# Optimization experiments

Measured on AMD Instinct MI355X. Metric: run time of the kernel, lower is better.

The kernel has to match this reference:

```python
import jax, jax.numpy as jnp
import numpy as np

N_DIST, H, W, K = 256, 256, 192, 129
DR, DR0, DELTA = 0.2, 0.2, 1e-11


def _dual_exp(d, b1, b2, b3, b4):
    return b1 * np.exp(-b2 * d) + b3 * np.exp(-b4 * d)


def setup_inputs() -> dict:
    key = jax.random.key(0)
    d = (np.arange(N_DIST) + 1.0) * DR                      # distances (cm)
    gaus_amp = _dual_exp(d, 1.0, 0.01, 0.1, 0.001)
    gaus_sig = 0.05 * d + 1.0
    bkg_amp = _dual_exp(d, 0.05, 0.05, 0.01, 0.005)
    bkg_sig = 0.08 * d + 2.0
    xk = np.arange(-(K // 2), K // 2 + 1) * DR / DR0        # (K,) kernel coords
    # gaussian kernel (get_gaus_layer)
    kernel_g = np.sqrt(gaus_amp)[:, None] * np.exp(-xk[None, :] ** 2 / (2 * gaus_sig[:, None] ** 2 + DELTA))
    # background kernels (get_bkg_layers) with emulated splines
    w_f = lambda t: np.exp(-np.abs(t))
    iso_f = lambda t: 1.0 / (1.0 + t ** 2)
    xw = xk[None, :] / bkg_sig[:, None]
    kernel_w = bkg_amp[:, None] * (DR / DR0) * w_f(xw)
    kernel_iso = bkg_amp[:, None] * (DR / DR0) * iso_f(xw)
    # normalization factor (configure)
    xs = np.linspace(-5.0, 5.0, 2001)
    Iw = np.trapz(w_f(xs), xs)
    Iiso = np.trapz(iso_f(xs), xs)
    Nw = 3 * bkg_amp * Iw * bkg_sig
    Niso = bkg_amp * Iiso * bkg_sig
    Ng2 = gaus_amp * 2 * np.pi * gaus_sig ** 2 * (DR0 / DR) ** 2
    norm = (Nw + Niso ** 2 + 1.0) * Ng2
    x = jax.random.uniform(key, (1, N_DIST, H, W), dtype=jnp.float32)
    return {
        "x": x,
        "kernel_g": jnp.asarray(kernel_g, jnp.float32),
        "kernel_w": jnp.asarray(kernel_w, jnp.float32),
        "kernel_iso": jnp.asarray(kernel_iso, jnp.float32),
        "norm": jnp.asarray(norm, jnp.float32),
    }


def _dwconv(x, kern, axis):
    """Depthwise 'same' Conv1d along `axis` of (N,H,W); channels = dim 0."""
    n = x.shape[0]
    perm = (2, 0, 1) if axis == 1 else (1, 0, 2)   # -> (batch, channels=N, length)
    inv = (1, 2, 0) if axis == 1 else (1, 0, 2)
    xb = jnp.transpose(x, perm)
    y = jax.lax.conv_general_dilated(
        xb, kern[:, None, :], (1,), 'SAME',
        feature_group_count=n, dimension_numbers=('NCH', 'OIH', 'NCH'))
    return jnp.transpose(y, inv)


def _rotate(x, ang):
    """Bilinear rotation of (N,S,S) in dims (1,2), zero padding (grid_sample-like)."""
    s = x.shape[1]
    c = (s - 1) * 0.5
    ca, sa = jnp.cos(ang), jnp.sin(ang)
    idx = jnp.arange(s, dtype=x.dtype) - c
    yy, xx = jnp.meshgrid(idx, idx, indexing='ij')
    sy = ca * yy + sa * xx + c   # inverse-rotated source coords
    sx = -sa * yy + ca * xx + c
    y0 = jnp.floor(sy)
    x0 = jnp.floor(sx)
    fy, fx = sy - y0, sx - x0
    y0i, x0i = y0.astype(jnp.int32), x0.astype(jnp.int32)

    def gat(yi, xi):
        valid = (yi >= 0) & (yi < s) & (xi >= 0) & (xi < s)
        v = x[:, jnp.clip(yi, 0, s - 1), jnp.clip(xi, 0, s - 1)]
        return jnp.where(valid, v, 0.0)

    return (gat(y0i, x0i) * (1 - fy) * (1 - fx)
            + gat(y0i, x0i + 1) * (1 - fy) * fx
            + gat(y0i + 1, x0i) * fy * (1 - fx)
            + gat(y0i + 1, x0i + 1) * fy * fx)


def reference(x, kernel_g, kernel_w, kernel_iso, norm):
    out = x[0]                                   # (N, H, W)
    out = _dwconv(out, kernel_g, 1)
    out = _dwconv(out, kernel_g, 2)
    iso = _dwconv(out, kernel_iso, 1)
    iso = _dwconv(iso, kernel_iso, 2)
    n, h, w = out.shape
    pad = (n - w) // 2
    padded = jnp.pad(out, ((0, 0), (0, 0), (pad, pad)))  # (N, H, H) square plane
    tails = jnp.zeros_like(padded)
    for i in range(3):                            # 0, 60, 120 degrees
        ang = float(np.deg2rad(60 * i))
        t = _rotate(padded, ang)
        t = _dwconv(t, kernel_w, 2)
        tails = tails + _rotate(t, -ang)
    tails = tails[:, :, pad:pad + w]
    out = (out + tails + iso) / norm[:, None, None]
    return out[None]
```

## Files before the change

kernel.cpp:

```cpp
#include <hip/hip_runtime.h>
#include <cmath>

#define CN   256
#define HN   256
#define WN   192
#define KN   129
#define RN   64
#define SN   256
#define PADN 32

#define BBR 92
#define BBP 96

template <int TW, int WD, bool ACC>
__global__ __launch_bounds__(512, 2) void conv_w_lds(const float* __restrict__ in,
                                                     const float* __restrict__ kern,
                                                     float* __restrict__ out) {
    constexpr int NO    = TW / 8;
    constexpr int TWW   = TW + 128;
    constexpr int PITCH = TWW + 1;
    constexpr int NB    = (2 * NO + 31) / NO;
    __shared__ float lds[64 * PITCH + 132];
    float* __restrict__ ldsK = lds + 64 * PITCH;
    const int tid = threadIdx.x;
    const int x0  = blockIdx.x * TW;
    const int h0  = blockIdx.y * 64;
    const int c   = blockIdx.z;
    const float* __restrict__ in_c = in + ((size_t)c * HN + h0) * WD;

    if (tid < 132) ldsK[tid] = (tid < KN) ? kern[c * KN + tid] : 0.f;

    const int colg = tid & 63;
    const int rr   = tid >> 6;
    const int off  = x0 - 64;

    if (off >= 0 && off + TWW <= WD) {
#pragma unroll
        for (int m = 0; m < 4; ++m) {
            if (colg + 64 * m < TWW) {
#pragma unroll
                for (int k = 0; k < 8; ++k)
                    lds[(rr + 8 * k) * PITCH + colg + 64 * m] =
                        in_c[(size_t)(rr + 8 * k) * WD + off + colg + 64 * m];
            }
        }
    } else {
#pragma unroll
        for (int m = 0; m < 4; ++m) {
            if (colg + 64 * m < TWW) {
#pragma unroll
                for (int k = 0; k < 8; ++k) {
                    int g  = off + colg + 64 * m;
                    int gc = min(max(g, 0), WD - 1);
                    float v = in_c[(size_t)(rr + 8 * k) * WD + gc];
                    lds[(rr + 8 * k) * PITCH + colg + 64 * m] = (g == gc) ? v : 0.f;
                }
            }
        }
    }
    __syncthreads();

    const int wv = tid >> 6;
    const int l  = tid & 63;
    const int base = l * PITCH + wv * NO;

    float acc[NO];
#pragma unroll
    for (int t = 0; t < NO; ++t) acc[t] = 0.f;

    float H[4][NO];
    const float4* __restrict__ k4 = (const float4*)ldsK;
#pragma unroll
    for (int s = 0; s < 4; ++s) {
        const int sb = base + 32 * s;
#pragma unroll
        for (int k = 0; k < NB - 1; ++k)
#pragma unroll
            for (int i = 0; i < NO; ++i) H[k][i] = lds[sb + k * NO + i];
        float4 kc = k4[8 * s];
#pragma unroll
        for (int q = 0; q < 8; ++q) {
            float4 kn = (q < 7) ? k4[8 * s + q + 1] : kc;
#pragma unroll
            for (int u = 0; u < 4; ++u) {
                const int up = 4 * q + u;
                const float kj = (u == 0) ? kc.x : (u == 1) ? kc.y
                               : (u == 2) ? kc.z : kc.w;
#pragma unroll
                for (int t = 0; t < NO; ++t) {
                    const int e = up + t;
                    const float val = (e < NO)     ? H[0][e]
                                    : (e < 2 * NO) ? H[1][e - NO]
                                    : (e < 3 * NO) ? H[2][e - 2 * NO]
                                                   : H[3][e - 3 * NO];
                    acc[t] = fmaf(val, kj, acc[t]);
                }
            }
            if (q == 0) {
#pragma unroll
                for (int i = 0; i < NO; ++i)
                    H[NB - 1][i] = lds[sb + (NB - 1) * NO + i];
            }
            kc = kn;
        }
        if (s == 3) {
            const float k128 = ldsK[128];
#pragma unroll
            for (int t = 0; t < NO; ++t) {
                const int e = 32 + t;
                const float val = (e < NO)     ? H[0][e]
                                : (e < 2 * NO) ? H[1][e - NO]
                                : (e < 3 * NO) ? H[2][e - 2 * NO]
                                               : H[3][e - 3 * NO];
                acc[t] = fmaf(val, k128, acc[t]);
            }
        }
    }

    __syncthreads();
#pragma unroll
    for (int i = 0; i < NO; ++i) lds[base + i] = acc[i];
    __syncthreads();
    float* __restrict__ obase = out + ((size_t)c * HN + h0) * WD + x0;
#pragma unroll
    for (int k = 0; k < (64 * TW) / 512; ++k) {
        const int idx = k * 512 + tid;
        const int r  = idx / TW;
        const int cl = idx - r * TW;
        float v = lds[r * PITCH + cl];
        if (ACC) v += obase[(size_t)r * WD + cl];
        obase[(size_t)r * WD + cl] = v;
    }
}

__global__ __launch_bounds__(512, 2) void conv_h_lds(const float* __restrict__ in,
                                                     const float* __restrict__ kern,
                                                     float* __restrict__ out) {
    __shared__ float lds[256 * 64 + 132];
    float* __restrict__ ldsK = lds + 256 * 64;
    const int tid = threadIdx.x;
    const int x0  = blockIdx.x * 64;
    const int h0  = blockIdx.y * 128;
    const int c   = blockIdx.z;
    const float* __restrict__ in_c = in + (size_t)c * HN * WN + x0;

    if (tid < 132) ldsK[tid] = (tid < KN) ? kern[c * KN + tid] : 0.f;

    {
        const int f4 = (tid & 15) * 4;
        const int rw = tid >> 4;
        const int off = h0 - 64;
#pragma unroll
        for (int p = 0; p < 8; ++p) {
            const int lr = rw + 32 * p;
            const int g  = off + lr;
            const int gc = min(max(g, 0), HN - 1);
            float4 v = *(const float4*)(in_c + (size_t)gc * WN + f4);
            if (g != gc) { v.x = 0.f; v.y = 0.f; v.z = 0.f; v.w = 0.f; }
            *(float4*)(lds + lr * 64 + f4) = v;
        }
    }
    __syncthreads();

    const int W = (tid >> 6) * 16;
    const int l = tid & 63;

    float acc[16];
#pragma unroll
    for (int t = 0; t < 16; ++t) acc[t] = 0.f;

    float X0[16], X1[16], X2[16], X3[16];

#define RD16(BUF, b)                                                          \
    { _Pragma("unroll")                                                       \
      for (int i = 0; i < 16; ++i) BUF[i] = lds[(W + 16 * (b) + i) * 64 + l]; }

#define STG(s, LOW, MID, HIGH, NXT, hasNxt)                                   \
    {                                                                         \
        const float4* __restrict__ k4 = (const float4*)ldsK;                  \
        float4 kc = k4[8 * (s)];                                              \
        _Pragma("unroll")                                                     \
        for (int q = 0; q < 8; ++q) {                                         \
            float4 kn = (q < 7) ? k4[8 * (s) + q + 1] : kc;                   \
            _Pragma("unroll")                                                 \
            for (int u = 0; u < 4; ++u) {                                     \
                const float kj = (u == 0) ? kc.x : (u == 1) ? kc.y            \
                               : (u == 2) ? kc.z : kc.w;                      \
                _Pragma("unroll")                                             \
                for (int t = 0; t < 16; ++t) {                                \
                    const int e = 4 * q + u + t;                              \
                    const float val = (e < 16) ? LOW[e]                       \
                                    : (e < 32) ? MID[e - 16] : HIGH[e - 32];  \
                    acc[t] = fmaf(val, kj, acc[t]);                           \
                }                                                             \
            }                                                                 \
            if (q == 0) RD16(HIGH, 2 * (s) + 2)                               \
            if ((hasNxt) && q == 1) RD16(NXT, 2 * (s) + 3)                    \
            kc = kn;                                                          \
        }                                                                     \
    }

    RD16(X0, 0)
    RD16(X1, 1)
    STG(0, X0, X1, X2, X3, true)
    STG(1, X2, X3, X0, X1, true)
    STG(2, X0, X1, X2, X3, true)
    STG(3, X2, X3, X0, X1, false)
#undef RD16
#undef STG

    {
        const float k128 = ldsK[128];
#pragma unroll
        for (int t = 0; t < 16; ++t) acc[t] = fmaf(X0[t], k128, acc[t]);
    }

    float* __restrict__ ob = out + ((size_t)c * HN + h0 + W) * WN + x0 + l;
#pragma unroll
    for (int t = 0; t < 16; ++t) ob[(size_t)t * WN] = acc[t];
}

__global__ __launch_bounds__(256) void rot_fwd_lds(const float* __restrict__ Cin,
                                                   float* __restrict__ out,
                                                   float ca, float sa) {
    __shared__ float tile[BBR * BBP];
    const int j0 = blockIdx.x * 64;
    const int i0 = blockIdx.y * 64;
    const int c  = blockIdx.z;
    const float cc = (SN - 1) * 0.5f;
    const float yA = (float)i0 - cc, yB = (float)(i0 + 63) - cc;
    const float xA = (float)j0 - cc, xB = (float)(j0 + 63) - cc;
    const float syAA = ca * yA + sa * xA + cc, syAB = ca * yA + sa * xB + cc;
    const float syBA = ca * yB + sa * xA + cc, syBB = ca * yB + sa * xB + cc;
    const float sxAA = -sa * yA + ca * xA + cc, sxAB = -sa * yA + ca * xB + cc;
    const float sxBA = -sa * yB + ca * xA + cc, sxBB = -sa * yB + ca * xB + cc;
    const int ybase = (int)floorf(fminf(fminf(syAA, syAB), fminf(syBA, syBB))) - 1;
    const int xbase = (int)floorf(fminf(fminf(sxAA, sxAB), fminf(sxBA, sxBB))) - 1;

    const float* __restrict__ base = Cin + (size_t)c * HN * WN;
    for (int t = threadIdx.x; t < BBR * BBP; t += 256) {
        const int r  = t / BBP;
        const int q  = t - r * BBP;
        const int gy = ybase + r;
        const int gx = xbase + q - PADN;
        float v = 0.f;
        if ((unsigned)gy < (unsigned)HN && (unsigned)gx < (unsigned)WN)
            v = base[(size_t)gy * WN + gx];
        tile[t] = v;
    }
    __syncthreads();

    const int l  = threadIdx.x & 63;
    const int r0 = threadIdx.x >> 6;
    const int j  = j0 + l;
    const float xx = (float)j - cc;
    float* __restrict__ ocol = out + (size_t)c * SN * SN + j;
#pragma unroll
    for (int t = 0; t < 16; ++t) {
        const int i = i0 + r0 + 4 * t;
        const float yy = (float)i - cc;
        const float sy = ca * yy + sa * xx + cc;
        const float sx = -sa * yy + ca * xx + cc;
        const float y0f = floorf(sy), x0f = floorf(sx);
        const float fy = sy - y0f, fx = sx - x0f;
        const int ly = (int)y0f - ybase;
        const int lx = (int)x0f - xbase;
        const float* p = tile + ly * BBP + lx;
        const float v00 = p[0], v01 = p[1], v10 = p[BBP], v11 = p[BBP + 1];
        ocol[(size_t)i * SN] = (1.f - fy) * ((1.f - fx) * v00 + fx * v01)
                             + fy * ((1.f - fx) * v10 + fx * v11);
    }
}

template <bool FINAL>
__global__ __launch_bounds__(256) void rot_bwd_lds(const float* __restrict__ U,
                                                   float* __restrict__ dst,
                                                   const float* __restrict__ accIn,
                                                   const float* __restrict__ norm,
                                                   float ca, float sa) {
    __shared__ float tile[BBR * BBP];
    const int x0 = blockIdx.x * 64;
    const int i0 = blockIdx.y * 64;
    const int c  = blockIdx.z;
    const float cc = (SN - 1) * 0.5f;
    const float yA = (float)i0 - cc, yB = (float)(i0 + 63) - cc;
    const float xA = (float)(x0 + PADN) - cc, xB = (float)(x0 + PADN + 63) - cc;
    const float syAA = ca * yA + sa * xA + cc, syAB = ca * yA + sa * xB + cc;
    const float syBA = ca * yB + sa * xA + cc, syBB = ca * yB + sa * xB + cc;
    const float sxAA = -sa * yA + ca * xA + cc, sxAB = -sa * yA + ca * xB + cc;
    const float sxBA = -sa * yB + ca * xA + cc, sxBB = -sa * yB + ca * xB + cc;
    const int ybase = (int)floorf(fminf(fminf(syAA, syAB), fminf(syBA, syBB))) - 1;
    const int xbase = (int)floorf(fminf(fminf(sxAA, sxAB), fminf(sxBA, sxBB))) - 1;

    const float* __restrict__ base = U + (size_t)c * SN * SN;
    for (int t = threadIdx.x; t < BBR * BBP; t += 256) {
        const int r  = t / BBP;
        const int q  = t - r * BBP;
        const int gy = ybase + r;
        const int gx = xbase + q;
        float v = 0.f;
        if ((unsigned)gy < (unsigned)SN && (unsigned)gx < (unsigned)SN)
            v = base[(size_t)gy * SN + gx];
        tile[t] = v;
    }
    __syncthreads();

    const int l  = threadIdx.x & 63;
    const int r0 = threadIdx.x >> 6;
    const int xc = x0 + l;
    const float xx = (float)(xc + PADN) - cc;
    float inv = 0.f;
    if constexpr (FINAL) inv = 1.f / norm[c];
#pragma unroll
    for (int t = 0; t < 16; ++t) {
        const int i = i0 + r0 + 4 * t;
        const float yy = (float)i - cc;
        const float sy = ca * yy + sa * xx + cc;
        const float sx = -sa * yy + ca * xx + cc;
        const float y0f = floorf(sy), x0f = floorf(sx);
        const float fy = sy - y0f, fx = sx - x0f;
        const int ly = (int)y0f - ybase;
        const int lx = (int)x0f - xbase;
        const float* p = tile + ly * BBP + lx;
        const float v00 = p[0], v01 = p[1], v10 = p[BBP], v11 = p[BBP + 1];
        const float val = (1.f - fy) * ((1.f - fx) * v00 + fx * v01)
                        + fy * ((1.f - fx) * v10 + fx * v11);
        const size_t idx = ((size_t)c * HN + i) * WN + xc;
        if constexpr (FINAL) {
            dst[idx] = (dst[idx] + accIn[idx] + val) * inv;
        } else {
            dst[idx] += val;
        }
    }
}

extern "C" void kernel_launch(void* const* d_in, const int* in_sizes, int n_in,
                              void* d_out, int out_size, void* d_ws, size_t ws_size,
                              hipStream_t stream) {
    const float* x    = (const float*)d_in[0];
    const float* kg   = (const float*)d_in[1];
    const float* kw   = (const float*)d_in[2];
    const float* kiso = (const float*)d_in[3];
    const float* norm = (const float*)d_in[4];

    float* C = (float*)d_out;
    float* ws = (float*)d_ws;
    const size_t IMG = (size_t)CN * HN * WN;
    const size_t PSQ = (size_t)CN * SN * SN;
    float* B   = ws;
    float* acc = ws + IMG;
    float* T   = ws + 2 * IMG;
    float* U   = T + PSQ;

    const dim3 blk256(256);
    const dim3 blk512(512);
    const dim3 convHGrid(WN / 64, HN / 128, CN);
    const dim3 convW192Grid(2, HN / 64, CN);
    const dim3 convW256Grid(2, HN / 64, CN);
    const dim3 rotFGrid(SN / 64, SN / 64, CN);
    const dim3 rotBGrid(WN / 64, HN / 64, CN);

    conv_h_lds<<<convHGrid, blk512, 0, stream>>>(x, kg, B);
    conv_w_lds<96, WN, false><<<convW192Grid, blk512, 0, stream>>>(B, kg, C);
    conv_h_lds<<<convHGrid, blk512, 0, stream>>>(C, kiso, B);
    conv_w_lds<96, WN, false><<<convW192Grid, blk512, 0, stream>>>(B, kiso, acc);
    conv_w_lds<96, WN, true><<<convW192Grid, blk512, 0, stream>>>(C, kw, acc);
    const double a1 = 60.0 * M_PI / 180.0, a2 = 120.0 * M_PI / 180.0;
    const float c1 = (float)cos(a1), s1 = (float)sin(a1);
    const float c2 = (float)cos(a2), s2 = (float)sin(a2);

    rot_fwd_lds<<<rotFGrid, blk256, 0, stream>>>(C, T, c1, s1);
    conv_w_lds<128, SN, false><<<convW256Grid, blk512, 0, stream>>>(T, kw, U);
    rot_bwd_lds<false><<<rotBGrid, blk256, 0, stream>>>(U, acc, nullptr, nullptr, c1, -s1);

    rot_fwd_lds<<<rotFGrid, blk256, 0, stream>>>(C, T, c2, s2);
    conv_w_lds<128, SN, false><<<convW256Grid, blk512, 0, stream>>>(T, kw, U);
    rot_bwd_lds<true><<<rotBGrid, blk256, 0, stream>>>(U, C, acc, norm, c2, -s2);

    (void)in_sizes; (void)n_in; (void)out_size; (void)ws_size;
}
```

Measured before the change: 705.9 us.

## Restructure width conv into full-row tiles with sliding 8-wide register window

The width-direction depthwise conv now loads a fixed 192-column window per 64-row tile with float4 LDS stores. It handles zero padding at register-fill time rather than staging a halo, and streams input through an 8x8 rotating register window instead of reloading 4 blocks per kernel segment. The 192-wide image convs switch to one block covering the full width, halving the grid and eliminating redundant halo loads. Output writes and the accumulate path become float4. This trades fewer blocks and more register pressure for less LDS and global traffic.

```diff
diff --git a/kernel.cpp b/kernel.cpp
--- a/kernel.cpp
+++ b/kernel.cpp
@@ -17,9 +17,12 @@
                                                      const float* __restrict__ kern,
                                                      float* __restrict__ out) {
     constexpr int NO    = TW / 8;
-    constexpr int TWW   = TW + 128;
-    constexpr int PITCH = TWW + 1;
-    constexpr int NB    = (2 * NO + 31) / NO;
+    constexpr int NBLK  = (NO + 32) / 8;
+    constexpr int TOTB  = (NO + 128) / 8;
+    constexpr int RC    = 192;
+    constexpr int PITCH = 196;
+    static_assert(NO == 16 || NO == 24, "unsupported TW");
+    static_assert(TW == WD || 2 * TW == WD, "grid.x must be edge tiles only");
     __shared__ float lds[64 * PITCH + 132];
     float* __restrict__ ldsK = lds + 64 * PITCH;
     const int tid = threadIdx.x;
@@ -30,106 +33,114 @@
 
     if (tid < 132) ldsK[tid] = (tid < KN) ? kern[c * KN + tid] : 0.f;
 
-    const int colg = tid & 63;
-    const int rr   = tid >> 6;
-    const int off  = x0 - 64;
-
-    if (off >= 0 && off + TWW <= WD) {
-#pragma unroll
-        for (int m = 0; m < 4; ++m) {
-            if (colg + 64 * m < TWW) {
-#pragma unroll
-                for (int k = 0; k < 8; ++k)
-                    lds[(rr + 8 * k) * PITCH + colg + 64 * m] =
-                        in_c[(size_t)(rr + 8 * k) * WD + off + colg + 64 * m];
-            }
-        }
-    } else {
-#pragma unroll
-        for (int m = 0; m < 4; ++m) {
-            if (colg + 64 * m < TWW) {
-#pragma unroll
-                for (int k = 0; k < 8; ++k) {
-                    int g  = off + colg + 64 * m;
-                    int gc = min(max(g, 0), WD - 1);
-                    float v = in_c[(size_t)(rr + 8 * k) * WD + gc];
-                    lds[(rr + 8 * k) * PITCH + colg + 64 * m] = (g == gc) ? v : 0.f;
+    const int gc0 = max(0, x0 - 64);
+    {
+        const int srow = tid >> 3;
+        const int scg  = tid & 7;
+#pragma unroll
+        for (int m = 0; m < 6; ++m) {
+            const int c4 = scg + 8 * m;
+            *(float4*)(lds + srow * PITCH + 4 * c4) =
+                *(const float4*)(in_c + (size_t)srow * WD + gc0 + 4 * c4);
+        }
+    }
+    __syncthreads();
+
+    const int wv  = tid >> 6;
+    const int l   = tid & 63;
+    const int ac0 = x0 + wv * NO - 64;
+    const int lbase = l * PITCH + (ac0 - gc0);
+
+    float acc[NO];
+#pragma unroll
+    for (int t = 0; t < NO; ++t) acc[t] = 0.f;
+
+    float X[8][8];
+
+#define RD8(G)                                                                \
+    if ((G) < TOTB) {                                                         \
+        const int ac_ = ac0 + 8 * (G);                                        \
+        if (ac_ >= 0 && ac_ + 8 <= WD) {             \
+            const float4 a_ = *(const float4*)(lds + lbase + 8 * (G));        \
+            const float4 b_ = *(const float4*)(lds + lbase + 8 * (G) + 4);    \
+            X[(G) & 7][0] = a_.x; X[(G) & 7][1] = a_.y;                       \
+            X[(G) & 7][2] = a_.z; X[(G) & 7][3] = a_.w;                       \
+            X[(G) & 7][4] = b_.x; X[(G) & 7][5] = b_.y;                       \
+            X[(G) & 7][6] = b_.z; X[(G) & 7][7] = b_.w;                       \
+        } else {                                                              \
+            _Pragma("unroll")                                                 \
+            for (int i_ = 0; i_ < 8; ++i_) {                                  \
+                const int cc_ = ac_ + i_;                                     \
+                const int cl_ = min(max(cc_, 0), WD - 1);                     \
+                const float v_ = lds[l * PITCH + (cl_ - gc0)];                \
+                X[(G) & 7][i_] = (cc_ == cl_) ? v_ : 0.f;                     \
+            }                                                                 \
+        }                                                                     \
+    }
+
+    RD8(0) RD8(1) RD8(2) RD8(3) RD8(4) RD8(5)
+    if (NBLK == 7) { RD8(6) }
+
+    const float4* __restrict__ k4 = (const float4*)ldsK;
+#pragma unroll
+    for (int s = 0; s < 4; ++s) {
+        float4 kc = k4[8 * s];
+#pragma unroll
+        for (int q = 0; q < 8; ++q) {
+            float4 kn = (q < 7) ? k4[8 * s + q + 1] : kc;
+#pragma unroll
+            for (int u = 0; u < 4; ++u) {
+                const float kj = (u == 0) ? kc.x : (u == 1) ? kc.y
+                               : (u == 2) ? kc.z : kc.w;
+#pragma unroll
+                for (int t = 0; t < NO; ++t) {
+                    const int e = 4 * q + u + t;
+                    acc[t] = fmaf(X[(4 * s + e / 8) & 7][e & 7], kj, acc[t]);
                 }
             }
-        }
-    }
-    __syncthreads();
-
-    const int wv = tid >> 6;
-    const int l  = tid & 63;
-    const int base = l * PITCH + wv * NO;
-
-    float acc[NO];
-#pragma unroll
-    for (int t = 0; t < NO; ++t) acc[t] = 0.f;
-
-    float H[4][NO];
-    const float4* __restrict__ k4 = (const float4*)ldsK;
-#pragma unroll
-    for (int s = 0; s < 4; ++s) {
-        const int sb = base + 32 * s;
-#pragma unroll
-        for (int k = 0; k < NB - 1; ++k)
-#pragma unroll
-            for (int i = 0; i < NO; ++i) H[k][i] = lds[sb + k * NO + i];
-        float4 kc = k4[8 * s];
-#pragma unroll
-        for (int q = 0; q < 8; ++q) {
-            float4 kn = (q < 7) ? k4[8 * s + q + 1] : kc;
-#pragma unroll
-            for (int u = 0; u < 4; ++u) {
-                const int up = 4 * q + u;
-                const float kj = (u == 0) ? kc.x : (u == 1) ? kc.y
-                               : (u == 2) ? kc.z : kc.w;
-#pragma unroll
-                for (int t = 0; t < NO; ++t) {
-                    const int e = up + t;
-                    const float val = (e < NO)     ? H[0][e]
-                                    : (e < 2 * NO) ? H[1][e - NO]
-                                    : (e < 3 * NO) ? H[2][e - 2 * NO]
-                                                   : H[3][e - 3 * NO];
-                    acc[t] = fmaf(val, kj, acc[t]);
-                }
-            }
-            if (q == 0) {
-#pragma unroll
-                for (int i = 0; i < NO; ++i)
-                    H[NB - 1][i] = lds[sb + (NB - 1) * NO + i];
+            if (NO == 16) {
+                if (q == 0) { RD8(4 * s + 6) }
+                if (q == 1) { RD8(4 * s + 7) }
+                if (q == 2) { RD8(4 * s + 8) }
+                if (q == 4) { RD8(4 * s + 9) }
+            } else {
+                if (q == 0) { RD8(4 * s + 7) }
+                if (q == 2) { RD8(4 * s + 8) }
+                if (q == 4) { RD8(4 * s + 9) }
+                if (q == 6) { RD8(4 * s + 10) }
             }
             kc = kn;
         }
-        if (s == 3) {
-            const float k128 = ldsK[128];
-#pragma unroll
-            for (int t = 0; t < NO; ++t) {
-                const int e = 32 + t;
-                const float val = (e < NO)     ? H[0][e]
-                                : (e < 2 * NO) ? H[1][e - NO]
-                                : (e < 3 * NO) ? H[2][e - 2 * NO]
-                                               : H[3][e - 3 * NO];
-                acc[t] = fmaf(val, k128, acc[t]);
-            }
-        }
-    }
-
-    __syncthreads();
-#pragma unroll
-    for (int i = 0; i < NO; ++i) lds[base + i] = acc[i];
+    }
+    {
+        const float k128 = ldsK[128];
+#pragma unroll
+        for (int t = 0; t < NO; ++t) {
+            const int e = 32 + t;
+            acc[t] = fmaf(X[(12 + e / 8) & 7][e & 7], k128, acc[t]);
+        }
+    }
+#undef RD8
+
+    __syncthreads();
+#pragma unroll
+    for (int i = 0; i < NO; i += 4)
+        *(float4*)(lds + l * PITCH + wv * NO + i) =
+            make_float4(acc[i], acc[i + 1], acc[i + 2], acc[i + 3]);
     __syncthreads();
     float* __restrict__ obase = out + ((size_t)c * HN + h0) * WD + x0;
-#pragma unroll
-    for (int k = 0; k < (64 * TW) / 512; ++k) {
-        const int idx = k * 512 + tid;
-        const int r  = idx / TW;
-        const int cl = idx - r * TW;
-        float v = lds[r * PITCH + cl];
-        if (ACC) v += obase[(size_t)r * WD + cl];
-        obase[(size_t)r * WD + cl] = v;
+    constexpr int NF4 = (64 * TW / 4) / 512;
+#pragma unroll
+    for (int k = 0; k < NF4; ++k) {
+        const int i4  = k * 512 + tid;
+        const int r   = i4 / (TW / 4);
+        const int c4o = i4 - r * (TW / 4);
+        float4 v = *(const float4*)(lds + r * PITCH + 4 * c4o);
+        if (ACC) {
+            const float4 o = *(const float4*)(obase + (size_t)r * WD + 4 * c4o);
+            v.x += o.x; v.y += o.y; v.z += o.z; v.w += o.w;
+        }
+        *(float4*)(obase + (size_t)r * WD + 4 * c4o) = v;
     }
 }
 
@@ -355,16 +366,16 @@
     const dim3 blk256(256);
     const dim3 blk512(512);
     const dim3 convHGrid(WN / 64, HN / 128, CN);
-    const dim3 convW192Grid(2, HN / 64, CN);
+    const dim3 convW192Grid(1, HN / 64, CN);
     const dim3 convW256Grid(2, HN / 64, CN);
     const dim3 rotFGrid(SN / 64, SN / 64, CN);
     const dim3 rotBGrid(WN / 64, HN / 64, CN);
 
     conv_h_lds<<<convHGrid, blk512, 0, stream>>>(x, kg, B);
-    conv_w_lds<96, WN, false><<<convW192Grid, blk512, 0, stream>>>(B, kg, C);
+    conv_w_lds<192, WN, false><<<convW192Grid, blk512, 0, stream>>>(B, kg, C);
     conv_h_lds<<<convHGrid, blk512, 0, stream>>>(C, kiso, B);
-    conv_w_lds<96, WN, false><<<convW192Grid, blk512, 0, stream>>>(B, kiso, acc);
-    conv_w_lds<96, WN, true><<<convW192Grid, blk512, 0, stream>>>(C, kw, acc);
+    conv_w_lds<192, WN, false><<<convW192Grid, blk512, 0, stream>>>(B, kiso, acc);
+    conv_w_lds<192, WN, true><<<convW192Grid, blk512, 0, stream>>>(C, kw, acc);
     const double a1 = 60.0 * M_PI / 180.0, a2 = 120.0 * M_PI / 180.0;
     const float c1 = (float)cos(a1), s1 = (float)sin(a1);
     const float c2 = (float)cos(a2), s2 = (float)sin(a2);
```

Measured after the change: 753.7 us. 1.07x slower.

## Add register-tiled width conv kernel for rotated 256-wide planes

Applied to the files above, without the earlier changes.

Adds a specialized depthwise conv kernel for the two 256-wide rotated-plane convolutions. Each thread keeps 16 outputs in registers and streams a rotating 6x8 window of inputs from LDS with float4 reads. It applies the kernel taps as outer-product style FMAs and raises launch bounds to 6 blocks per SM to improve occupancy. Outputs are staged back through LDS for coalesced float4 stores. The cost is higher register use and a kernel path hand-specialized for these sizes.

```diff
diff --git a/kernel.cpp b/kernel.cpp
--- a/kernel.cpp
+++ b/kernel.cpp
@@ -11,6 +11,117 @@
 
 #define BBR 92
 #define BBP 96
+
+template <int WD>
+__global__ __launch_bounds__(512, 6) void conv_w256(const float* __restrict__ in,
+                                                    const float* __restrict__ kern,
+                                                    float* __restrict__ out) {
+    constexpr int NO    = 16;
+    constexpr int TW    = 128;
+    constexpr int TOTB  = (NO + 128) / 8;
+    constexpr int PITCH = 196;
+    __shared__ float lds[64 * PITCH + 132];
+    float* __restrict__ ldsK = lds + 64 * PITCH;
+    const int tid = threadIdx.x;
+    const int x0  = blockIdx.x * TW;
+    const int h0  = blockIdx.y * 64;
+    const int c   = blockIdx.z;
+    const float* __restrict__ in_c = in + ((size_t)c * HN + h0) * WD;
+
+    if (tid < 132) ldsK[tid] = (tid < KN) ? kern[c * KN + tid] : 0.f;
+
+    const int gc0 = max(0, x0 - 64);
+    {
+        const int srow = tid >> 3;
+        const int scg  = tid & 7;
+#pragma unroll
+        for (int m = 0; m < 6; ++m) {
+            const int c4 = scg + 8 * m;
+            *(float4*)(lds + srow * PITCH + 4 * c4) =
+                *(const float4*)(in_c + (size_t)srow * WD + gc0 + 4 * c4);
+        }
+    }
+    __syncthreads();
+
+    const int wv  = tid >> 6;
+    const int l   = tid & 63;
+    const int ac0 = x0 + wv * NO - 64;
+    const int lbase = l * PITCH + (ac0 - gc0);
+
+    float acc[NO];
+#pragma unroll
+    for (int t = 0; t < NO; ++t) acc[t] = 0.f;
+
+    float X[6][8];
+
+#define RD8(G)                                                                \
+    if ((G) < TOTB) {                                                         \
+        const int ac_ = ac0 + 8 * (G);                                        \
+        if (ac_ >= 0 && ac_ < WD) {                                           \
+            const float4 a_ = *(const float4*)(lds + lbase + 8 * (G));        \
+            const float4 b_ = *(const float4*)(lds + lbase + 8 * (G) + 4);    \
+            X[(G) % 6][0] = a_.x; X[(G) % 6][1] = a_.y;                       \
+            X[(G) % 6][2] = a_.z; X[(G) % 6][3] = a_.w;                       \
+            X[(G) % 6][4] = b_.x; X[(G) % 6][5] = b_.y;                       \
+            X[(G) % 6][6] = b_.z; X[(G) % 6][7] = b_.w;                       \
+        } else {                                                              \
+            _Pragma("unroll")                                                 \
+            for (int i_ = 0; i_ < 8; ++i_) X[(G) % 6][i_] = 0.f;              \
+        }                                                                     \
+    }
+
+    RD8(0) RD8(1) RD8(2) RD8(3) RD8(4)
+
+    const float4* __restrict__ k4 = (const float4*)ldsK;
+#pragma unroll
+    for (int s = 0; s < 4; ++s) {
+        float4 kc = k4[8 * s];
+#pragma unroll
+        for (int q = 0; q < 8; ++q) {
+            float4 kn = (q < 7) ? k4[8 * s + q + 1] : kc;
+#pragma unroll
+            for (int u = 0; u < 4; ++u) {
+                const float kj = (u == 0) ? kc.x : (u == 1) ? kc.y
+                               : (u == 2) ? kc.z : kc.w;
+#pragma unroll
+                for (int t = 0; t < NO; ++t) {
+                    const int e = 4 * q + u + t;
+                    acc[t] = fmaf(X[(4 * s + e / 8) % 6][e % 8], kj, acc[t]);
+                }
+            }
+            if (q == 0) { RD8(4 * s + 5) }
+            if (q == 2) { RD8(4 * s + 6) }
+            if (q == 4) { RD8(4 * s + 7) }
+            if (q == 6) { RD8(4 * s + 8) }
+            kc = kn;
+        }
+    }
+    {
+        const float k128 = ldsK[128];
+#pragma unroll
+        for (int t = 0; t < NO; ++t) {
+            const int e = 32 + t;
+            acc[t] = fmaf(X[(12 + e / 8) % 6][e % 8], k128, acc[t]);
+        }
+    }
+#undef RD8
+
+    __syncthreads();
+#pragma unroll
+    for (int i = 0; i < NO; i += 4)
+        *(float4*)(lds + l * PITCH + wv * NO + i) =
+            make_float4(acc[i], acc[i + 1], acc[i + 2], acc[i + 3]);
+    __syncthreads();
+    float* __restrict__ obase = out + ((size_t)c * HN + h0) * WD + x0;
+#pragma unroll
+    for (int k = 0; k < 4; ++k) {
+        const int i4  = k * 512 + tid;
+        const int r   = i4 >> 5;
+        const int c4o = i4 & 31;
+        *(float4*)(obase + (size_t)r * WD + 4 * c4o) =
+            *(const float4*)(lds + r * PITCH + 4 * c4o);
+    }
+}
 
 template <int TW, int WD, bool ACC>
 __global__ __launch_bounds__(512, 2) void conv_w_lds(const float* __restrict__ in,
@@ -370,11 +481,11 @@
     const float c2 = (float)cos(a2), s2 = (float)sin(a2);
 
     rot_fwd_lds<<<rotFGrid, blk256, 0, stream>>>(C, T, c1, s1);
-    conv_w_lds<128, SN, false><<<convW256Grid, blk512, 0, stream>>>(T, kw, U);
+    conv_w256<SN><<<convW256Grid, blk512, 0, stream>>>(T, kw, U);
     rot_bwd_lds<false><<<rotBGrid, blk256, 0, stream>>>(U, acc, nullptr, nullptr, c1, -s1);
 
     rot_fwd_lds<<<rotFGrid, blk256, 0, stream>>>(C, T, c2, s2);
-    conv_w_lds<128, SN, false><<<convW256Grid, blk512, 0, stream>>>(T, kw, U);
+    conv_w256<SN><<<convW256Grid, blk512, 0, stream>>>(T, kw, U);
     rot_bwd_lds<true><<<rotBGrid, blk256, 0, stream>>>(U, C, acc, norm, c2, -s2);
 
     (void)in_sizes; (void)n_in; (void)out_size; (void)ws_size;
```

Measured after the change: 1.930 ms. +173.4%, slower.
